# Kernel optimization log

Hardware: AMD Instinct MI355X
Metric: run time of the kernel (lower is better)

The kernel has to match this reference:

```python
import jax, jax.numpy as jnp
import numpy as np

B, N, F_IN = 8, 1024, 25   # batch, num_edges (GAT nodes), features_per_link = 1 + 8*num_bands
H, D = 8, 16               # num_heads, output_dim per head (hidden_size // num_heads)
NEG_INF = -9e15            # matches torch -9000000000000000.0


def setup_inputs() -> dict:
    key = jax.random.key(0)
    k1, k2, k3, k4 = jax.random.split(key, 4)
    node_feats = jax.random.normal(k1, (B, N, F_IN), dtype=jnp.float32)
    adj = jax.random.randint(k2, (B, N, N), 0, 2, dtype=jnp.int32)
    # Xavier-uniform-ish params per GATLayer.reset_parameters (gain for relu)
    gain = float(np.sqrt(2.0))
    limW = gain * np.sqrt(6.0 / (F_IN + D))
    lima = gain * np.sqrt(6.0 / (2 * D + 1))
    W = jax.random.uniform(k3, (H, F_IN, D), jnp.float32, -limW, limW)
    a = jax.random.uniform(k4, (H, 2 * D, 1), jnp.float32, -lima, lima)
    return {"node_feats": node_feats, "adj": adj, "W": W, "a": a}


def reference(node_feats, adj, W, a):
    d = W.shape[-1]
    # Wh: [B, H, N, D]
    Wh = jnp.einsum('bnf,hfd->bhnd', node_feats, W)
    # Additive attention: e_ij = <Wh_i, a_src> + <Wh_j, a_dst>  (no LeakyReLU in this module)
    a_src = a[:, :d, 0]   # [H, D]
    a_dst = a[:, d:, 0]   # [H, D]
    ei = jnp.einsum('bhnd,hd->bhn', Wh, a_src)  # [B, H, N]
    ej = jnp.einsum('bhnd,hd->bhn', Wh, a_dst)  # [B, H, N]
    e = ei[:, :, :, None] + ej[:, :, None, :]   # [B, H, N, N]
    mask = adj[:, None, :, :].astype(bool)      # [B, 1->H, N, N]
    e = jnp.where(mask, e, jnp.asarray(NEG_INF, e.dtype))
    alpha = jax.nn.softmax(e, axis=-1)          # dropout is identity at eval
    h_prime = jnp.einsum('bhij,bhjd->bhid', alpha, Wh)        # [B, H, N, D]
    h_prime = h_prime.transpose(0, 2, 1, 3).reshape(node_feats.shape[0], node_feats.shape[1], -1)
    return jax.nn.relu(h_prime), alpha
```

## Files before the change

### kernel.cpp

```cpp
#include <hip/hip_runtime.h>

#define L2E 1.44269504f

typedef short short8_t  __attribute__((ext_vector_type(8)));
typedef float fltx4     __attribute__((ext_vector_type(4)));
typedef int   intx4     __attribute__((ext_vector_type(4)));
typedef unsigned short ushort4_t __attribute__((ext_vector_type(4)));
typedef unsigned int uint32;

__device__ __forceinline__ unsigned short f2bf(float f) {
    uint32 u = __float_as_uint(f);
    u += 0x7FFFu + ((u >> 16) & 1u);
    return (unsigned short)(u >> 16);
}

__global__ __launch_bounds__(256) void prep_once(
    const float* __restrict__ x,
    const float* __restrict__ W,
    const float* __restrict__ a,
    float* __restrict__ ej_ws,
    unsigned short* __restrict__ whb)
{
    int t  = blockIdx.x * 256 + threadIdx.x;
    int bh = t >> 10, n = t & 1023;
    int b  = bh >> 3, h = bh & 7;

    const float* xr = x + ((size_t)(b * 1024 + n)) * 25;
    const float* Wp = W + h * 400;
    const float* ap = a + h * 32;

    float xf[25];
    #pragma unroll
    for (int f = 0; f < 25; ++f) xf[f] = xr[f];

    int base = ((bh * 32 + (n >> 5)) * 64 + ((n >> 3) & 3) * 16) * 8 + (n & 7);
    float vj = 0.f;
    #pragma unroll
    for (int d = 0; d < 16; ++d) {
        float s = 0.f;
        #pragma unroll
        for (int f = 0; f < 25; ++f) s += xf[f] * Wp[f * 16 + d];
        vj += s * ap[16 + d];
        whb[base + d * 8] = f2bf(s);
    }
    ej_ws[t] = vj;
}

__global__ __launch_bounds__(256) void gat_main(
    const int*   __restrict__ adj,
    const float* __restrict__ ej_ws,
    const unsigned short* __restrict__ whb,
    float* __restrict__ out0,
    float* __restrict__ out1)
{
    __shared__ __align__(16) unsigned short palds[32 * 1024];

    const int blk   = blockIdx.x;
    const int x8    = blk & 7;
    const int h     = (blk >> 3) & 7;
    const int s     = blk >> 6;
    const int c     = s * 8 + x8;
    const int b     = c >> 5;
    const int chunk = c & 31;
    const int bh    = b * 8 + h;
    const int wave  = threadIdx.x >> 6;
    const int lane  = threadIdx.x & 63;
    const int i0    = chunk * 32;

    const fltx4* ej4 = (const fltx4*)(ej_ws + bh * 1024);
    fltx4 expr_[4];
    #pragma unroll
    for (int j0 = 0; j0 < 4; ++j0) {
        fltx4 e = ej4[j0 * 64 + lane];
        fltx4 r;
        r.x = exp2f(e.x * L2E); r.y = exp2f(e.y * L2E);
        r.z = exp2f(e.z * L2E); r.w = exp2f(e.w * L2E);
        expr_[j0] = r;
    }

    float* abase = out1 + (size_t)bh * 1024 * 1024;
    char*  ldsb  = (char*)palds;

    const intx4* adjb = (const intx4*)(adj + ((size_t)b * 1024 + i0 + wave * 8) * 1024);
    intx4 av[8][4];
    #pragma unroll
    for (int r = 0; r < 8; ++r)
        #pragma unroll
        for (int j0 = 0; j0 < 4; ++j0)
            av[r][j0] = adjb[r * 256 + j0 * 64 + lane];

    float sum[8];
    #pragma unroll
    for (int r = 0; r < 8; ++r) {
        float s0 = 0.f;
        #pragma unroll
        for (int j0 = 0; j0 < 4; ++j0) {
            intx4 a4 = av[r][j0];
            fltx4 ev = expr_[j0];
            s0 += (a4.x ? ev.x : 0.f) + (a4.y ? ev.y : 0.f)
                + (a4.z ? ev.z : 0.f) + (a4.w ? ev.w : 0.f);
        }
        sum[r] = s0;
    }

    #pragma unroll
    for (int off = 32; off; off >>= 1) {
        #pragma unroll
        for (int r = 0; r < 8; ++r) sum[r] += __shfl_xor(sum[r], off);
    }

    #pragma unroll
    for (int r = 0; r < 8; ++r) {
        const int rl = wave * 8 + r;
        const int i  = i0 + rl;
        const bool ok = sum[r] > 0.f;
        const float rinv = ok ? __builtin_amdgcn_rcpf(sum[r]) : 0.f;
        const float fb   = ok ? 0.f : (1.0f / 1024.0f);

        float* arow = abase + (size_t)i * 1024;
        const int swz  = (rl & 7) << 4;
        char* lrow = ldsb + rl * 2048;
        #pragma unroll
        for (int j0 = 0; j0 < 4; ++j0) {
            intx4 a4 = av[r][j0];
            fltx4 ev = expr_[j0];
            fltx4 st;
            st.x = a4.x ? ev.x * rinv + fb : fb;
            st.y = a4.y ? ev.y * rinv + fb : fb;
            st.z = a4.z ? ev.z * rinv + fb : fb;
            st.w = a4.w ? ev.w * rinv + fb : fb;
            __builtin_nontemporal_store(st, (fltx4*)(arow + (j0 * 64 + lane) * 4));
            ushort4_t bv;
            bv.x = f2bf(st.x); bv.y = f2bf(st.y);
            bv.z = f2bf(st.z); bv.w = f2bf(st.w);
            *(ushort4_t*)(lrow + (((j0 * 512) + lane * 8) ^ swz)) = bv;
        }
    }

    __syncthreads();

    if (wave < 2) {
        const int mrow = lane & 15;
        const int quad = lane >> 4;
        const int rl   = wave * 16 + mrow;
        const int swz  = (rl & 7) << 4;
        char* lrow = ldsb + rl * 2048;
        const unsigned short* bbase = whb + (size_t)bh * 16384;

        fltx4 acc = {0.f, 0.f, 0.f, 0.f};
        #pragma unroll 4
        for (int ks = 0; ks < 32; ++ks) {
            short8_t afr = *(const short8_t*)(lrow + ((ks * 64 + quad * 16) ^ swz));
            short8_t bfr = *(const short8_t*)(bbase + ((ks * 64 + lane) << 3));
            acc = __builtin_amdgcn_mfma_f32_16x16x32_bf16(afr, bfr, acc, 0, 0, 0);
        }

        #pragma unroll
        for (int r = 0; r < 4; ++r) {
            int i = i0 + wave * 16 + quad * 4 + r;
            float v = acc[r] > 0.f ? acc[r] : 0.f;
            out0[((size_t)(b * 1024 + i)) * 128 + h * 16 + mrow] = v;
        }
    }
}

__global__ __launch_bounds__(256) void gat_fused(
    const float* __restrict__ x, const int* __restrict__ adj,
    const float* __restrict__ W, const float* __restrict__ a,
    float* __restrict__ out0, float* __restrict__ out1)
{
    __shared__ __align__(16) unsigned short whb[32 * 64 * 8];
    __shared__ __align__(16) float ej_lds[1024];
    __shared__ float ei_lds[64];
    __shared__ float wa[64];

    const int bh    = blockIdx.x >> 4;
    const int chunk = blockIdx.x & 15;
    const int b     = bh >> 3;
    const int h     = bh & 7;
    const int tid   = threadIdx.x;
    const int wave  = tid >> 6;
    const int lane  = tid & 63;
    const int mrow  = lane & 15;
    const int quad  = lane >> 4;

    const float* Wp = W + h * 400;
    const float* ap = a + h * 32;
    const float* xb = x + (size_t)b * 1024 * 25;

    if (tid < 50) {
        int f = tid % 25, which = tid / 25;
        float s = 0.f;
        #pragma unroll
        for (int d = 0; d < 16; ++d) s += Wp[f * 16 + d] * ap[which * 16 + d];
        wa[which * 32 + f] = s;
    }
    __syncthreads();

    for (int s = 0; s < 4; ++s) {
        int n = tid + (s << 8);
        const float* xr = xb + n * 25;
        float xf[25];
        #pragma unroll
        for (int f = 0; f < 25; ++f) xf[f] = xr[f];
        float vi = 0.f, vj = 0.f;
        #pragma unroll
        for (int f = 0; f < 25; ++f) { vi += xf[f] * wa[f]; vj += xf[f] * wa[32 + f]; }
        ej_lds[n] = vj;
        if ((n >> 6) == chunk) ei_lds[n & 63] = vi;
        int base = (((n >> 5) * 64 + ((n >> 3) & 3) * 16) << 3) + (n & 7);
        #pragma unroll
        for (int d = 0; d < 16; ++d) {
            float s2 = 0.f;
            #pragma unroll
            for (int f = 0; f < 25; ++f) s2 += xf[f] * Wp[f * 16 + d];
            whb[base + d * 8] = f2bf(s2);
        }
    }
    __syncthreads();

    const int i0 = chunk * 64 + wave * 16;
    float* abase = out1 + (size_t)bh * 1024 * 1024;
    const fltx4* ej4 = (const fltx4*)ej_lds;

    for (int r = 0; r < 16; ++r) {
        int i = i0 + r;
        float s_ei = ei_lds[wave * 16 + r];
        const intx4* adj4 = (const intx4*)(adj + ((size_t)b * 1024 + i) * 1024);
        float p[16];
        float sum = 0.f;
        #pragma unroll
        for (int j0 = 0; j0 < 4; ++j0) {
            intx4 av = adj4[j0 * 64 + lane];
            fltx4 ev = ej4[j0 * 64 + lane];
            float p0 = av.x ? exp2f((s_ei + ev.x) * L2E) : 0.f;
            float p1 = av.y ? exp2f((s_ei + ev.y) * L2E) : 0.f;
            float p2 = av.z ? exp2f((s_ei + ev.z) * L2E) : 0.f;
            float p3 = av.w ? exp2f((s_ei + ev.w) * L2E) : 0.f;
            p[j0 * 4 + 0] = p0; p[j0 * 4 + 1] = p1;
            p[j0 * 4 + 2] = p2; p[j0 * 4 + 3] = p3;
            sum += (p0 + p1) + (p2 + p3);
        }
        #pragma unroll
        for (int off = 32; off; off >>= 1) sum += __shfl_xor(sum, off);
        float rinv;
        if (sum > 0.f) {
            rinv = __builtin_amdgcn_rcpf(sum);
        } else {
            rinv = 1.0f;
            #pragma unroll
            for (int k = 0; k < 16; ++k) p[k] = 1.0f / 1024.0f;
        }
        float* arow = abase + (size_t)i * 1024;
        #pragma unroll
        for (int j0 = 0; j0 < 4; ++j0) {
            fltx4 st;
            st.x = p[j0 * 4 + 0] * rinv; st.y = p[j0 * 4 + 1] * rinv;
            st.z = p[j0 * 4 + 2] * rinv; st.w = p[j0 * 4 + 3] * rinv;
            *(fltx4*)(arow + (j0 * 64 + lane) * 4) = st;
        }
    }

    __builtin_amdgcn_fence(__ATOMIC_ACQ_REL, "workgroup");

    const float* aptr = abase + (size_t)(i0 + mrow) * 1024 + quad * 8;
    fltx4 acc = {0.f, 0.f, 0.f, 0.f};
    for (int ks = 0; ks < 32; ++ks) {
        fltx4 a0 = *(const fltx4*)(aptr + ks * 32);
        fltx4 a1 = *(const fltx4*)(aptr + ks * 32 + 4);
        short8_t afr;
        #pragma unroll
        for (int q = 0; q < 4; ++q) {
            afr[q]     = (short)f2bf(a0[q]);
            afr[4 + q] = (short)f2bf(a1[q]);
        }
        short8_t bfr = *(const short8_t*)&whb[((ks * 64 + lane) << 3)];
        acc = __builtin_amdgcn_mfma_f32_16x16x32_bf16(afr, bfr, acc, 0, 0, 0);
    }
    #pragma unroll
    for (int r = 0; r < 4; ++r) {
        int i = i0 + quad * 4 + r;
        float v = acc[r] > 0.f ? acc[r] : 0.f;
        out0[((size_t)(b * 1024 + i)) * 128 + h * 16 + mrow] = v;
    }
}

extern "C" void kernel_launch(void* const* d_in, const int* in_sizes, int n_in,
                              void* d_out, int out_size, void* d_ws, size_t ws_size,
                              hipStream_t stream) {
    const float* x   = (const float*)d_in[0];
    const int*   adj = (const int*)d_in[1];
    const float* W   = (const float*)d_in[2];
    const float* a   = (const float*)d_in[3];

    float* out0 = (float*)d_out;
    float* out1 = out0 + (size_t)8 * 1024 * 128;

    const size_t WHB_BYTES = (size_t)64 * 16384 * 2;
    const size_t EJ_BYTES  = (size_t)64 * 1024 * 4;
    const size_t NEED      = WHB_BYTES + EJ_BYTES;

    if (ws_size >= NEED) {
        unsigned short* whb = (unsigned short*)d_ws;
        float* ej_ws = (float*)((char*)d_ws + WHB_BYTES);
        prep_once<<<256, 256, 0, stream>>>(x, W, a, ej_ws, whb);
        gat_main<<<2048, 256, 0, stream>>>(adj, ej_ws, whb, out0, out1);
    } else {
        gat_fused<<<1024, 256, 0, stream>>>(x, adj, W, a, out0, out1);
    }
}
```

Measured before the change: 315.0 us.

## Halve rows per block, bit-pack adjacency mask, precompute exp in prep

Each gat_main block now handles 16 rows instead of 32, so the grid doubles to 4096 blocks and LDS per block halves. Adjacency values are packed into a 16-bit mask per row instead of being held as 32 int vectors in registers. The exp of ej is computed once in prep_once rather than in every block. Together these cut register and LDS pressure to raise occupancy and drop redundant exp work. In exchange, each whb/ej tile is reloaded by twice as many blocks and only one wave per block does the MFMA step.

```diff
diff --git a/kernel.cpp b/kernel.cpp
--- a/kernel.cpp
+++ b/kernel.cpp
@@ -18,7 +18,7 @@
     const float* __restrict__ x,
     const float* __restrict__ W,
     const float* __restrict__ a,
-    float* __restrict__ ej_ws,
+    float* __restrict__ pexp_ws,
     unsigned short* __restrict__ whb)
 {
     int t  = blockIdx.x * 256 + threadIdx.x;
@@ -43,62 +43,66 @@
         vj += s * ap[16 + d];
         whb[base + d * 8] = f2bf(s);
     }
-    ej_ws[t] = vj;
+    pexp_ws[t] = exp2f(vj * L2E);
 }
 
 __global__ __launch_bounds__(256) void gat_main(
     const int*   __restrict__ adj,
-    const float* __restrict__ ej_ws,
+    const float* __restrict__ pexp_ws,
     const unsigned short* __restrict__ whb,
     float* __restrict__ out0,
     float* __restrict__ out1)
 {
-    __shared__ __align__(16) unsigned short palds[32 * 1024];
+    __shared__ __align__(16) unsigned short palds[16 * 1024];
 
     const int blk   = blockIdx.x;
     const int x8    = blk & 7;
     const int h     = (blk >> 3) & 7;
     const int s     = blk >> 6;
     const int c     = s * 8 + x8;
-    const int b     = c >> 5;
-    const int chunk = c & 31;
+    const int b     = c >> 6;
+    const int chunk = c & 63;
     const int bh    = b * 8 + h;
     const int wave  = threadIdx.x >> 6;
     const int lane  = threadIdx.x & 63;
-    const int i0    = chunk * 32;
-
-    const fltx4* ej4 = (const fltx4*)(ej_ws + bh * 1024);
+    const int i0    = chunk * 16;
+
+    const fltx4* pe4 = (const fltx4*)(pexp_ws + bh * 1024);
     fltx4 expr_[4];
     #pragma unroll
-    for (int j0 = 0; j0 < 4; ++j0) {
-        fltx4 e = ej4[j0 * 64 + lane];
-        fltx4 r;
-        r.x = exp2f(e.x * L2E); r.y = exp2f(e.y * L2E);
-        r.z = exp2f(e.z * L2E); r.w = exp2f(e.w * L2E);
-        expr_[j0] = r;
-    }
+    for (int j0 = 0; j0 < 4; ++j0) expr_[j0] = pe4[j0 * 64 + lane];
 
     float* abase = out1 + (size_t)bh * 1024 * 1024;
     char*  ldsb  = (char*)palds;
 
-    const intx4* adjb = (const intx4*)(adj + ((size_t)b * 1024 + i0 + wave * 8) * 1024);
-    intx4 av[8][4];
-    #pragma unroll
-    for (int r = 0; r < 8; ++r)
-        #pragma unroll
-        for (int j0 = 0; j0 < 4; ++j0)
-            av[r][j0] = adjb[r * 256 + j0 * 64 + lane];
-
-    float sum[8];
-    #pragma unroll
-    for (int r = 0; r < 8; ++r) {
+    const intx4* adjb = (const intx4*)(adj + ((size_t)b * 1024 + i0 + wave * 4) * 1024);
+    uint32 msk[4];
+    #pragma unroll
+    for (int r = 0; r < 4; ++r) {
+        uint32 m = 0;
+        #pragma unroll
+        for (int j0 = 0; j0 < 4; ++j0) {
+            intx4 a4 = adjb[r * 256 + j0 * 64 + lane];
+            m |= (a4.x ? (1u << (j0 * 4 + 0)) : 0u);
+            m |= (a4.y ? (1u << (j0 * 4 + 1)) : 0u);
+            m |= (a4.z ? (1u << (j0 * 4 + 2)) : 0u);
+            m |= (a4.w ? (1u << (j0 * 4 + 3)) : 0u);
+        }
+        msk[r] = m;
+    }
+
+    float sum[4];
+    #pragma unroll
+    for (int r = 0; r < 4; ++r) {
         float s0 = 0.f;
-        #pragma unroll
-        for (int j0 = 0; j0 < 4; ++j0) {
-            intx4 a4 = av[r][j0];
+        const uint32 m = msk[r];
+        #pragma unroll
+        for (int j0 = 0; j0 < 4; ++j0) {
             fltx4 ev = expr_[j0];
-            s0 += (a4.x ? ev.x : 0.f) + (a4.y ? ev.y : 0.f)
-                + (a4.z ? ev.z : 0.f) + (a4.w ? ev.w : 0.f);
+            s0 += ((m >> (j0 * 4 + 0)) & 1u) ? ev.x : 0.f;
+            s0 += ((m >> (j0 * 4 + 1)) & 1u) ? ev.y : 0.f;
+            s0 += ((m >> (j0 * 4 + 2)) & 1u) ? ev.z : 0.f;
+            s0 += ((m >> (j0 * 4 + 3)) & 1u) ? ev.w : 0.f;
         }
         sum[r] = s0;
     }
@@ -106,13 +110,14 @@
     #pragma unroll
     for (int off = 32; off; off >>= 1) {
         #pragma unroll
-        for (int r = 0; r < 8; ++r) sum[r] += __shfl_xor(sum[r], off);
-    }
-
-    #pragma unroll
-    for (int r = 0; r < 8; ++r) {
-        const int rl = wave * 8 + r;
+        for (int r = 0; r < 4; ++r) sum[r] += __shfl_xor(sum[r], off);
+    }
+
+    #pragma unroll
+    for (int r = 0; r < 4; ++r) {
+        const int rl = wave * 4 + r;
         const int i  = i0 + rl;
+        const uint32 m = msk[r];
         const bool ok = sum[r] > 0.f;
         const float rinv = ok ? __builtin_amdgcn_rcpf(sum[r]) : 0.f;
         const float fb   = ok ? 0.f : (1.0f / 1024.0f);
@@ -122,13 +127,12 @@
         char* lrow = ldsb + rl * 2048;
         #pragma unroll
         for (int j0 = 0; j0 < 4; ++j0) {
-            intx4 a4 = av[r][j0];
             fltx4 ev = expr_[j0];
             fltx4 st;
-            st.x = a4.x ? ev.x * rinv + fb : fb;
-            st.y = a4.y ? ev.y * rinv + fb : fb;
-            st.z = a4.z ? ev.z * rinv + fb : fb;
-            st.w = a4.w ? ev.w * rinv + fb : fb;
+            st.x = ((m >> (j0 * 4 + 0)) & 1u) ? ev.x * rinv + fb : fb;
+            st.y = ((m >> (j0 * 4 + 1)) & 1u) ? ev.y * rinv + fb : fb;
+            st.z = ((m >> (j0 * 4 + 2)) & 1u) ? ev.z * rinv + fb : fb;
+            st.w = ((m >> (j0 * 4 + 3)) & 1u) ? ev.w * rinv + fb : fb;
             __builtin_nontemporal_store(st, (fltx4*)(arow + (j0 * 64 + lane) * 4));
             ushort4_t bv;
             bv.x = f2bf(st.x); bv.y = f2bf(st.y);
@@ -139,12 +143,11 @@
 
     __syncthreads();
 
-    if (wave < 2) {
+    if (wave == 0) {
         const int mrow = lane & 15;
         const int quad = lane >> 4;
-        const int rl   = wave * 16 + mrow;
-        const int swz  = (rl & 7) << 4;
-        char* lrow = ldsb + rl * 2048;
+        const int swz  = (mrow & 7) << 4;
+        char* lrow = ldsb + mrow * 2048;
         const unsigned short* bbase = whb + (size_t)bh * 16384;
 
         fltx4 acc = {0.f, 0.f, 0.f, 0.f};
@@ -157,7 +160,7 @@
 
         #pragma unroll
         for (int r = 0; r < 4; ++r) {
-            int i = i0 + wave * 16 + quad * 4 + r;
+            int i = i0 + quad * 4 + r;
             float v = acc[r] > 0.f ? acc[r] : 0.f;
             out0[((size_t)(b * 1024 + i)) * 128 + h * 16 + mrow] = v;
         }
@@ -302,9 +305,9 @@
 
     if (ws_size >= NEED) {
         unsigned short* whb = (unsigned short*)d_ws;
-        float* ej_ws = (float*)((char*)d_ws + WHB_BYTES);
-        prep_once<<<256, 256, 0, stream>>>(x, W, a, ej_ws, whb);
-        gat_main<<<2048, 256, 0, stream>>>(adj, ej_ws, whb, out0, out1);
+        float* pexp_ws = (float*)((char*)d_ws + WHB_BYTES);
+        prep_once<<<256, 256, 0, stream>>>(x, W, a, pexp_ws, whb);
+        gat_main<<<4096, 256, 0, stream>>>(adj, pexp_ws, whb, out0, out1);
     } else {
         gat_fused<<<1024, 256, 0, stream>>>(x, adj, W, a, out0, out1);
     }
```

Result: slower. 322.3 us (+2.3%).
